# Performance work log

Measured on AMD Instinct MI355X. Metric: run time of the kernel, lower is better.

The kernel has to match this reference:

```python
import jax, jax.numpy as jnp
import numpy as np

N = 64        # n_nodes per graph
H = 128       # hidden channels (128x0e + 128x1o)
NB = 8        # radial bessel basis size
L = 2         # num_interactions
R_MAX = 5.0
AVG_NEIGH = 63.0
DIM = 3       # output vector dim
B = 64        # batch (vmapped)
T = 32        # time-embedding dim
S = 5         # num_species


def _edges(n):
    # fully-connected graph, no self loops (static shapes, jit-friendly)
    s, r = np.meshgrid(np.arange(n), np.arange(n), indexing='ij')
    m = s != r
    return jnp.asarray(s[m]), jnp.asarray(r[m])


def setup_inputs() -> dict:
    key = jax.random.key(0)
    ks = jax.random.split(key, 12)
    sc = 0.05
    return {
        'positions': jax.random.normal(ks[0], (B, N, 3), jnp.float32),
        'node_features': jax.random.randint(ks[1], (B, N), 0, S).astype(jnp.int64),
        'global_features': jax.random.normal(ks[2], (B, T), jnp.float32),
        'emb': jax.random.normal(ks[3], (S, H), jnp.float32) * sc,
        'Wt': jax.random.normal(ks[4], (T, H), jnp.float32) * sc,
        'Wr1': jax.random.normal(ks[5], (L, NB, H), jnp.float32) * sc,
        'Wr2': jax.random.normal(ks[6], (L, H, H), jnp.float32) * sc,
        'Wupd': jax.random.normal(ks[7], (L, H, H), jnp.float32) * sc,
        'Wmix': jax.random.normal(ks[8], (L, H, H), jnp.float32) * sc,
        'Wg1': jax.random.normal(ks[9], (H, H), jnp.float32) * sc,
        'Wg2': jax.random.normal(ks[10], (H, H), jnp.float32) * sc,
        'final_scaling': jnp.ones((), jnp.float32),
    }


def _call_single(pos, z, t, emb, Wt, Wr1, Wr2, Wupd, Wmix, Wg1, Wg2, final_scaling):
    snd, rcv = _edges(N)
    ev = pos[rcv] - pos[snd]                               # [E,3] edge vectors (gather)
    r = jnp.sqrt(jnp.sum(ev * ev, axis=-1) + 1e-12)        # [E]
    u = ev / r[:, None]                                    # unit directions
    # Bessel radial basis with cosine cutoff (r_max acts as soft radius graph)
    n = jnp.arange(1, NB + 1, dtype=pos.dtype)
    rb = jnp.sin(n * jnp.pi * r[:, None] / R_MAX) / r[:, None]   # [E,NB]
    fc = 0.5 * (jnp.cos(jnp.pi * r / R_MAX) + 1.0) * (r < R_MAX)
    rb = rb * fc[:, None]
    # node embedding from species + time embedding
    h = emb[z] + t @ Wt                                    # [N,H] scalar features
    v = jnp.zeros((N, H, DIM), pos.dtype)                  # vector (1o) features
    for l in range(L):
        w = jax.nn.silu(rb @ Wr1[l]) @ Wr2[l]              # [E,H] radial weights
        m0 = w * h[snd]                                    # [E,H] scalar messages
        m1 = m0[:, :, None] * u[:, None, :]                # [E,H,3] vector messages
        a0 = jax.ops.segment_sum(m0, rcv, num_segments=N) / AVG_NEIGH
        a1 = jax.ops.segment_sum(m1, rcv, num_segments=N) / AVG_NEIGH
        h = h + a0 @ Wupd[l]
        v = v + jnp.einsum('ngd,gh->nhd', a1, Wmix[l])
    # equivariant readout: scalar gate per channel contracts vector channels
    g = jax.nn.silu(h @ Wg1) @ Wg2                         # [N,H]
    out = jnp.einsum('nhd,nh->nd', v, g)                   # [N,3]
    return out * final_scaling


def reference(positions, node_features, global_features, emb, Wt, Wr1, Wr2, Wupd, Wmix, Wg1, Wg2, final_scaling):
    f = lambda p, z, t: _call_single(p, z, t, emb, Wt, Wr1, Wr2, Wupd, Wmix, Wg1, Wg2, final_scaling)
    return jax.vmap(f)(positions, node_features, global_features)
```

## Files before the change

### kernel.cpp

```cpp
#include <hip/hip_runtime.h>
#include <math.h>

#define NN 64
#define HH 128
#define NBB 8
#define TT 32
#define BB 64
#define NROW (BB * NN)
#define PLANE ((size_t)NROW * HH)
#define WR1OFF (8 * 16384)

typedef __attribute__((ext_vector_type(8))) short short8;
typedef __attribute__((ext_vector_type(4))) float f32x4;
typedef __attribute__((ext_vector_type(2))) float f32x2;

__device__ __forceinline__ float silu_f(float x) {
  return x * __builtin_amdgcn_rcpf(1.0f + __expf(-x));
}

__device__ __forceinline__ unsigned short f2bf(float x) {
  union { float f; unsigned u; } v; v.f = x;
  unsigned r = v.u + 0x7FFFu + ((v.u >> 16) & 1u);
  return (unsigned short)(r >> 16);
}

__device__ __forceinline__ void gemm16(
    const unsigned short (*sA)[136], const unsigned short* __restrict__ Bp,
    int w, int nlo, int quad, f32x4 C[2]) {
  short8 afr[4];
#pragma unroll
  for (int kt = 0; kt < 4; ++kt)
    afr[kt] = *(const short8*)&sA[nlo][kt * 32 + quad * 8];
#pragma unroll
  for (int nt = 0; nt < 2; ++nt)
#pragma unroll
    for (int kt = 0; kt < 4; ++kt) {
      short8 bfr = *(const short8*)&Bp[((kt * 128 + w * 32 + nt * 16 + nlo) * 4 + quad) * 8];
      C[nt] = __builtin_amdgcn_mfma_f32_16x16x32_bf16(afr[kt], bfr, C[nt], 0, 0, 0);
    }
}

__global__ __launch_bounds__(256) void k_init(
    const float* __restrict__ emb, const int* __restrict__ z,
    const float* __restrict__ gf, const float* __restrict__ Wt,
    const float* __restrict__ Wr1, const float* __restrict__ Wr2,
    const float* __restrict__ Wupd, const float* __restrict__ Wmix,
    const float* __restrict__ Wg1, const float* __restrict__ Wg2,
    float* __restrict__ h, unsigned short* __restrict__ Wpack) {
  __shared__ float tvec[HH];
  __shared__ int sz[NN];
  int b = blockIdx.x, tid = threadIdx.x;
#pragma unroll
  for (int ii = 0; ii < 8; ++ii) {
    int idx = b * 2048 + ii * 256 + tid;
    int m = idx >> 14;
    int local = idx & 16383;
    float val;
    if (m < 2) val = Wr2[idx];
    else if (m < 4) val = Wupd[idx - 32768];
    else if (m < 6) val = Wmix[idx - 65536];
    else if (m == 6) val = Wg1[local];
    else val = Wg2[local];
    int k = local >> 7, n = local & 127;
    int kt = k >> 5, q = (k >> 3) & 3, j = k & 7;
    Wpack[(idx & ~16383) + (((kt * 128 + n) * 4 + q) * 8) + j] = f2bf(val);
  }
  if (tid < 128) {
    int e = b * 128 + tid;
    int l = e >> 12, p = e & 4095;
    int n = p >> 5, q = (p >> 3) & 3, j = p & 7;
    float val = (q == 0) ? Wr1[l * NBB * HH + j * HH + n] : 0.f;
    Wpack[WR1OFF + l * 4096 + p] = f2bf(val);
  }
  if (tid < NN) sz[tid] = z[b * NN + tid];
  if (tid < HH) {
    float acc = 0.f;
#pragma unroll
    for (int k = 0; k < TT; ++k) acc += gf[b * TT + k] * Wt[k * HH + tid];
    tvec[tid] = acc;
  }
  __syncthreads();
  for (int i = tid; i < NN * HH; i += 256) {
    int n = i >> 7, c = i & 127;
    h[(size_t)b * NN * HH + i] = emb[sz[n] * HH + c] + tvec[c];
  }
}

__global__ __launch_bounds__(256) void k_layer(
    const float* __restrict__ pos,
    const float* __restrict__ hin,
    float* __restrict__ ap,
    const unsigned short* __restrict__ Wpack,
    int l) {
  __shared__ __align__(16) unsigned short sh_S[2][NN][136];
  __shared__ __align__(16) unsigned short sh_rbh[2][NN][8];
  __shared__ __align__(16) float sh_u[2][3][NN];

  int blk = blockIdx.x;
  int b = blk >> 5, rp = blk & 31;
  int r0 = rp * 2;
  int tid = threadIdx.x;
  int w = tid >> 6, lane = tid & 63;
  int nlo = lane & 15, quad = lane >> 4;
  const float* hb = hin + (size_t)b * NN * HH;

  float hbv[4][2][4];
#pragma unroll
  for (int mt = 0; mt < 4; ++mt)
#pragma unroll
    for (int nt = 0; nt < 2; ++nt)
#pragma unroll
      for (int reg = 0; reg < 4; ++reg)
        hbv[mt][nt][reg] = hb[(mt * 16 + quad * 4 + reg) * HH + w * 32 + nt * 16 + nlo];

  {
    int s = tid & 63;
    int ksel = (tid >> 6) & 1;
    int ri = (tid >> 7) & 1;
    int r = r0 + ri;
    const float* pb = pos + b * NN * 3;
    float dx = pb[r * 3 + 0] - pb[s * 3 + 0];
    float dy = pb[r * 3 + 1] - pb[s * 3 + 1];
    float dz = pb[r * 3 + 2] - pb[s * 3 + 2];
    float rr = sqrtf(dx * dx + dy * dy + dz * dz + 1e-12f);
    float inv = __builtin_amdgcn_rcpf(rr);
    if (ksel == 0) {
      sh_u[ri][0][s] = dx * inv; sh_u[ri][1][s] = dy * inv; sh_u[ri][2][s] = dz * inv;
    }
    const float PI_OVER_5 = 0.628318530717958647692f;
    float fc = (s != r && rr < 5.0f) ? 0.5f * (__cosf(PI_OVER_5 * rr) + 1.0f) : 0.0f;
    float base = PI_OVER_5 * rr;
    float sc = inv * fc;
    int k0 = ksel * 4;
    float v0 = __sinf((float)(k0 + 1) * base) * sc;
    float v1 = __sinf((float)(k0 + 2) * base) * sc;
    float v2 = __sinf((float)(k0 + 3) * base) * sc;
    float v3 = __sinf((float)(k0 + 4) * base) * sc;
    *(unsigned*)&sh_rbh[ri][s][k0]     = (unsigned)f2bf(v0) | ((unsigned)f2bf(v1) << 16);
    *(unsigned*)&sh_rbh[ri][s][k0 + 2] = (unsigned)f2bf(v2) | ((unsigned)f2bf(v3) << 16);
  }
  __syncthreads();

  {
    const unsigned short* Wr1p = Wpack + WR1OFF + l * 4096;
    short8 bw[2];
#pragma unroll
    for (int nt = 0; nt < 2; ++nt)
      bw[nt] = *(const short8*)&Wr1p[((w * 32 + nt * 16 + nlo) * 4 + quad) * 8];
    const short8 zero8 = {0, 0, 0, 0, 0, 0, 0, 0};
#pragma unroll
    for (int ri = 0; ri < 2; ++ri)
#pragma unroll
      for (int mtp = 0; mtp < 2; ++mtp) {
        f32x4 Cs[2][2];
#pragma unroll
        for (int mi = 0; mi < 2; ++mi)
#pragma unroll
          for (int nt = 0; nt < 2; ++nt) Cs[mi][nt] = (f32x4){0.f, 0.f, 0.f, 0.f};
#pragma unroll
        for (int mi = 0; mi < 2; ++mi) {
          int mt = mtp * 2 + mi;
          short8 afr = (quad == 0) ? *(const short8*)&sh_rbh[ri][mt * 16 + nlo][0] : zero8;
#pragma unroll
          for (int nt = 0; nt < 2; ++nt)
            Cs[mi][nt] = __builtin_amdgcn_mfma_f32_16x16x32_bf16(afr, bw[nt], Cs[mi][nt], 0, 0, 0);
        }
#pragma unroll
        for (int mi = 0; mi < 2; ++mi)
#pragma unroll
          for (int nt = 0; nt < 2; ++nt)
#pragma unroll
            for (int reg = 0; reg < 4; ++reg) {
              int s = (mtp * 2 + mi) * 16 + quad * 4 + reg;
              int c = w * 32 + nt * 16 + nlo;
              sh_S[ri][s][c] = f2bf(silu_f(Cs[mi][nt][reg]));
            }
      }
  }
  __syncthreads();

  const unsigned short* Bbase = Wpack + l * 16384;
  short8 bfr[4][2];
#pragma unroll
  for (int kt = 0; kt < 4; ++kt)
#pragma unroll
    for (int nt = 0; nt < 2; ++nt)
      bfr[kt][nt] = *(const short8*)&Bbase[((kt * 128 + w * 32 + nt * 16 + nlo) * 4 + quad) * 8];

  const float invAvg = 1.0f / 63.0f;
#pragma unroll
  for (int ri = 0; ri < 2; ++ri) {
    float acc0[2] = {0.f, 0.f};
    float a1x[2] = {0.f, 0.f};
    float a1y[2] = {0.f, 0.f};
    float a1z[2] = {0.f, 0.f};
#pragma unroll
    for (int mt = 0; mt < 4; ++mt) {
      short8 afr[4];
      int s_a = mt * 16 + nlo;
#pragma unroll
      for (int kt = 0; kt < 4; ++kt)
        afr[kt] = *(const short8*)&sh_S[ri][s_a][kt * 32 + quad * 8];
      float ux[4], uy[4], uz[4];
#pragma unroll
      for (int reg = 0; reg < 4; ++reg) {
        int s = mt * 16 + quad * 4 + reg;
        ux[reg] = sh_u[ri][0][s]; uy[reg] = sh_u[ri][1][s]; uz[reg] = sh_u[ri][2][s];
      }
#pragma unroll
      for (int nt = 0; nt < 2; ++nt) {
        f32x4 C = {0.f, 0.f, 0.f, 0.f};
#pragma unroll
        for (int kt = 0; kt < 4; ++kt)
          C = __builtin_amdgcn_mfma_f32_16x16x32_bf16(afr[kt], bfr[kt][nt], C, 0, 0, 0);
#pragma unroll
        for (int reg = 0; reg < 4; ++reg) {
          float m0 = C[reg] * hbv[mt][nt][reg];
          acc0[nt] += m0;
          a1x[nt] += m0 * ux[reg];
          a1y[nt] += m0 * uy[reg];
          a1z[nt] += m0 * uz[reg];
        }
      }
    }
#pragma unroll
    for (int nt = 0; nt < 2; ++nt) {
      float q0 = acc0[nt], q1 = a1x[nt], q2 = a1y[nt], q3 = a1z[nt];
      q0 += __shfl_xor(q0, 16); q0 += __shfl_xor(q0, 32);
      q1 += __shfl_xor(q1, 16); q1 += __shfl_xor(q1, 32);
      q2 += __shfl_xor(q2, 16); q2 += __shfl_xor(q2, 32);
      q3 += __shfl_xor(q3, 16); q3 += __shfl_xor(q3, 32);
      if (quad == 0) {
        size_t base = (size_t)(b * NN + r0 + ri) * HH + w * 32 + nt * 16 + nlo;
        ap[base]             = q0 * invAvg;
        ap[PLANE + base]     = q1 * invAvg;
        ap[2 * PLANE + base] = q2 * invAvg;
        ap[3 * PLANE + base] = q3 * invAvg;
      }
    }
  }
}

__global__ __launch_bounds__(256) void k_update(
    const float* __restrict__ ap, const float* __restrict__ hin,
    float* __restrict__ hout, float* __restrict__ vp,
    const unsigned short* __restrict__ Wpack) {
  __shared__ __align__(16) unsigned short sh_a[4][16][136];
  int tid = threadIdx.x, w = tid >> 6, lane = tid & 63;
  int nlo = lane & 15, quad = lane >> 4;
  int row0 = blockIdx.x * 16;
#pragma unroll
  for (int p = 0; p < 4; ++p)
#pragma unroll
    for (int ii = 0; ii < 4; ++ii) {
      int i = ii * 256 + tid;
      int rr = i >> 6, c2 = (i & 63) * 2;
      f32x2 t = *(const f32x2*)&ap[p * PLANE + (size_t)(row0 + rr) * HH + c2];
      *(unsigned*)&sh_a[p][rr][c2] = (unsigned)f2bf(t.x) | ((unsigned)f2bf(t.y) << 16);
    }
  __syncthreads();
  f32x4 Ch[2] = {{0,0,0,0},{0,0,0,0}}, Cx[2] = {{0,0,0,0},{0,0,0,0}};
  f32x4 Cy[2] = {{0,0,0,0},{0,0,0,0}}, Cz[2] = {{0,0,0,0},{0,0,0,0}};
  gemm16(sh_a[0], Wpack + 2 * 16384, w, nlo, quad, Ch);
  gemm16(sh_a[1], Wpack + 4 * 16384, w, nlo, quad, Cx);
  gemm16(sh_a[2], Wpack + 4 * 16384, w, nlo, quad, Cy);
  gemm16(sh_a[3], Wpack + 4 * 16384, w, nlo, quad, Cz);
#pragma unroll
  for (int nt = 0; nt < 2; ++nt)
#pragma unroll
    for (int reg = 0; reg < 4; ++reg) {
      size_t row = row0 + quad * 4 + reg;
      int col = w * 32 + nt * 16 + nlo;
      hout[row * HH + col] = hin[row * HH + col] + Ch[nt][reg];
      vp[0 * PLANE + row * HH + col] = Cx[nt][reg];
      vp[1 * PLANE + row * HH + col] = Cy[nt][reg];
      vp[2 * PLANE + row * HH + col] = Cz[nt][reg];
    }
}

__global__ __launch_bounds__(256) void k_update_ro(
    const float* __restrict__ ap, const float* __restrict__ hin,
    const float* __restrict__ vp,
    const unsigned short* __restrict__ Wpack,
    const float* __restrict__ fs, float* __restrict__ out) {
  __shared__ __align__(16) unsigned short sh_a[4][16][136];
  __shared__ __align__(16) unsigned short sh_h[16][136];
  __shared__ float red[4][16][3];
  int tid = threadIdx.x, w = tid >> 6, lane = tid & 63;
  int nlo = lane & 15, quad = lane >> 4;
  int row0 = blockIdx.x * 16;
#pragma unroll
  for (int p = 0; p < 4; ++p)
#pragma unroll
    for (int ii = 0; ii < 4; ++ii) {
      int i = ii * 256 + tid;
      int rr = i >> 6, c2 = (i & 63) * 2;
      f32x2 t = *(const f32x2*)&ap[p * PLANE + (size_t)(row0 + rr) * HH + c2];
      *(unsigned*)&sh_a[p][rr][c2] = (unsigned)f2bf(t.x) | ((unsigned)f2bf(t.y) << 16);
    }
  __syncthreads();
  f32x4 Ch[2] = {{0,0,0,0},{0,0,0,0}}, Cx[2] = {{0,0,0,0},{0,0,0,0}};
  f32x4 Cy[2] = {{0,0,0,0},{0,0,0,0}}, Cz[2] = {{0,0,0,0},{0,0,0,0}};
  gemm16(sh_a[0], Wpack + 3 * 16384, w, nlo, quad, Ch);
  gemm16(sh_a[1], Wpack + 5 * 16384, w, nlo, quad, Cx);
  gemm16(sh_a[2], Wpack + 5 * 16384, w, nlo, quad, Cy);
  gemm16(sh_a[3], Wpack + 5 * 16384, w, nlo, quad, Cz);
#pragma unroll
  for (int nt = 0; nt < 2; ++nt)
#pragma unroll
    for (int reg = 0; reg < 4; ++reg) {
      int rl = quad * 4 + reg;
      size_t row = row0 + rl;
      int col = w * 32 + nt * 16 + nlo;
      sh_h[rl][col] = f2bf(hin[row * HH + col] + Ch[nt][reg]);
      Cx[nt][reg] += vp[0 * PLANE + row * HH + col];
      Cy[nt][reg] += vp[1 * PLANE + row * HH + col];
      Cz[nt][reg] += vp[2 * PLANE + row * HH + col];
    }
  __syncthreads();
  unsigned short (*sh_q)[136] = sh_a[0];
  f32x4 Cq[2] = {{0,0,0,0},{0,0,0,0}};
  gemm16(sh_h, Wpack + 6 * 16384, w, nlo, quad, Cq);
#pragma unroll
  for (int nt = 0; nt < 2; ++nt)
#pragma unroll
    for (int reg = 0; reg < 4; ++reg)
      sh_q[quad * 4 + reg][w * 32 + nt * 16 + nlo] = f2bf(silu_f(Cq[nt][reg]));
  __syncthreads();
  f32x4 Cg[2] = {{0,0,0,0},{0,0,0,0}};
  gemm16(sh_q, Wpack + 7 * 16384, w, nlo, quad, Cg);
  float pr[3][4];
#pragma unroll
  for (int d = 0; d < 3; ++d)
#pragma unroll
    for (int reg = 0; reg < 4; ++reg) pr[d][reg] = 0.f;
#pragma unroll
  for (int nt = 0; nt < 2; ++nt)
#pragma unroll
    for (int reg = 0; reg < 4; ++reg) {
      float gv = Cg[nt][reg];
      pr[0][reg] += gv * Cx[nt][reg];
      pr[1][reg] += gv * Cy[nt][reg];
      pr[2][reg] += gv * Cz[nt][reg];
    }
#pragma unroll
  for (int off = 1; off < 16; off <<= 1)
#pragma unroll
    for (int d = 0; d < 3; ++d)
#pragma unroll
      for (int reg = 0; reg < 4; ++reg)
        pr[d][reg] += __shfl_xor(pr[d][reg], off);
  if (nlo == 0) {
#pragma unroll
    for (int d = 0; d < 3; ++d)
#pragma unroll
      for (int reg = 0; reg < 4; ++reg)
        red[w][quad * 4 + reg][d] = pr[d][reg];
  }
  __syncthreads();
  if (tid < 48) {
    int row = tid / 3, d = tid % 3;
    float s = red[0][row][d] + red[1][row][d] + red[2][row][d] + red[3][row][d];
    out[(size_t)(row0 + row) * 3 + d] = s * fs[0];
  }
}

extern "C" void kernel_launch(void* const* d_in, const int* in_sizes, int n_in,
                              void* d_out, int out_size, void* d_ws, size_t ws_size,
                              hipStream_t stream) {
  const float* pos  = (const float*)d_in[0];
  const int*   z    = (const int*)d_in[1];
  const float* gf   = (const float*)d_in[2];
  const float* emb  = (const float*)d_in[3];
  const float* Wt   = (const float*)d_in[4];
  const float* Wr1  = (const float*)d_in[5];
  const float* Wr2  = (const float*)d_in[6];
  const float* Wupd = (const float*)d_in[7];
  const float* Wmix = (const float*)d_in[8];
  const float* Wg1  = (const float*)d_in[9];
  const float* Wg2  = (const float*)d_in[10];
  const float* fs   = (const float*)d_in[11];
  float* out = (float*)d_out;

  float* ws = (float*)d_ws;
  float* hA = ws;
  float* hB = ws + PLANE;
  float* vp = ws + 2 * PLANE;
  float* apl = ws + 5 * PLANE;
  unsigned short* Wpack = (unsigned short*)(ws + 9 * PLANE);

  k_init<<<dim3(BB), dim3(256), 0, stream>>>(emb, z, gf, Wt, Wr1, Wr2, Wupd,
                                             Wmix, Wg1, Wg2, hA, Wpack);
  k_layer<<<dim3(BB * 32), dim3(256), 0, stream>>>(pos, hA, apl, Wpack, 0);
  k_update<<<dim3(256), dim3(256), 0, stream>>>(apl, hA, hB, vp, Wpack);
  k_layer<<<dim3(BB * 32), dim3(256), 0, stream>>>(pos, hB, apl, Wpack, 1);
  k_update_ro<<<dim3(256), dim3(256), 0, stream>>>(apl, hB, vp, Wpack, fs, out);
}
```

Measured before the change: 155.6 us.

## Eliminate intermediate update kernel by recomputing h in layer and deferring vector mix

Removes the k_update launch. The layer-1 kernel now recomputes h = hA + a0·Wupd0 per block with MFMA from bf16 layer-0 aggregates. The layer-0 vector mix is deferred to the final readout, which sums both layers' Wmix contributions by linearity. Aggregates are stored as bf16 instead of fp32, halving that traffic and dropping the fp32 v-plane round trip. The cost is redundant recomputation of the 64x128x128 h-update in each of the 32 blocks per graph, plus extra bf16 rounding of aggregates.

```diff
diff --git a/kernel.cpp b/kernel.cpp
--- a/kernel.cpp
+++ b/kernel.cpp
@@ -88,8 +88,9 @@
 
 __global__ __launch_bounds__(256) void k_layer(
     const float* __restrict__ pos,
-    const float* __restrict__ hin,
-    float* __restrict__ ap,
+    const float* __restrict__ hA,
+    const unsigned short* __restrict__ a0in,
+    unsigned short* __restrict__ apout,
     const unsigned short* __restrict__ Wpack,
     int l) {
   __shared__ __align__(16) unsigned short sh_S[2][NN][136];
@@ -102,16 +103,16 @@
   int tid = threadIdx.x;
   int w = tid >> 6, lane = tid & 63;
   int nlo = lane & 15, quad = lane >> 4;
-  const float* hb = hin + (size_t)b * NN * HH;
-
-  float hbv[4][2][4];
+
+  f32x4 hbv[4][2];
 #pragma unroll
   for (int mt = 0; mt < 4; ++mt)
 #pragma unroll
     for (int nt = 0; nt < 2; ++nt)
 #pragma unroll
       for (int reg = 0; reg < 4; ++reg)
-        hbv[mt][nt][reg] = hb[(mt * 16 + quad * 4 + reg) * HH + w * 32 + nt * 16 + nlo];
+        hbv[mt][nt][reg] =
+            hA[((size_t)b * NN + mt * 16 + quad * 4 + reg) * HH + w * 32 + nt * 16 + nlo];
 
   {
     int s = tid & 63;
@@ -139,7 +140,33 @@
     *(unsigned*)&sh_rbh[ri][s][k0]     = (unsigned)f2bf(v0) | ((unsigned)f2bf(v1) << 16);
     *(unsigned*)&sh_rbh[ri][s][k0 + 2] = (unsigned)f2bf(v2) | ((unsigned)f2bf(v3) << 16);
   }
-  __syncthreads();
+  if (l) {
+    for (int i = tid; i < NN * 64; i += 256) {
+      int s = i >> 6, c2 = (i & 63) * 2;
+      *(unsigned*)&sh_S[0][s][c2] =
+          *(const unsigned*)&a0in[((size_t)b * NN + s) * HH + c2];
+    }
+  }
+  __syncthreads();
+
+  if (l) {
+    const unsigned short* Bu = Wpack + 2 * 16384;
+#pragma unroll
+    for (int mt = 0; mt < 4; ++mt) {
+      short8 afr[4];
+#pragma unroll
+      for (int kt = 0; kt < 4; ++kt)
+        afr[kt] = *(const short8*)&sh_S[0][mt * 16 + nlo][kt * 32 + quad * 8];
+#pragma unroll
+      for (int nt = 0; nt < 2; ++nt)
+#pragma unroll
+        for (int kt = 0; kt < 4; ++kt) {
+          short8 bfr = *(const short8*)&Bu[((kt * 128 + w * 32 + nt * 16 + nlo) * 4 + quad) * 8];
+          hbv[mt][nt] = __builtin_amdgcn_mfma_f32_16x16x32_bf16(afr[kt], bfr, hbv[mt][nt], 0, 0, 0);
+        }
+    }
+    __syncthreads();
+  }
 
   {
     const unsigned short* Wr1p = Wpack + WR1OFF + l * 4096;
@@ -232,91 +259,57 @@
       q3 += __shfl_xor(q3, 16); q3 += __shfl_xor(q3, 32);
       if (quad == 0) {
         size_t base = (size_t)(b * NN + r0 + ri) * HH + w * 32 + nt * 16 + nlo;
-        ap[base]             = q0 * invAvg;
-        ap[PLANE + base]     = q1 * invAvg;
-        ap[2 * PLANE + base] = q2 * invAvg;
-        ap[3 * PLANE + base] = q3 * invAvg;
+        apout[(l * 4 + 0) * PLANE + base] = f2bf(q0 * invAvg);
+        apout[(l * 4 + 1) * PLANE + base] = f2bf(q1 * invAvg);
+        apout[(l * 4 + 2) * PLANE + base] = f2bf(q2 * invAvg);
+        apout[(l * 4 + 3) * PLANE + base] = f2bf(q3 * invAvg);
       }
     }
   }
 }
 
-__global__ __launch_bounds__(256) void k_update(
-    const float* __restrict__ ap, const float* __restrict__ hin,
-    float* __restrict__ hout, float* __restrict__ vp,
-    const unsigned short* __restrict__ Wpack) {
-  __shared__ __align__(16) unsigned short sh_a[4][16][136];
-  int tid = threadIdx.x, w = tid >> 6, lane = tid & 63;
-  int nlo = lane & 15, quad = lane >> 4;
-  int row0 = blockIdx.x * 16;
-#pragma unroll
-  for (int p = 0; p < 4; ++p)
-#pragma unroll
-    for (int ii = 0; ii < 4; ++ii) {
-      int i = ii * 256 + tid;
-      int rr = i >> 6, c2 = (i & 63) * 2;
-      f32x2 t = *(const f32x2*)&ap[p * PLANE + (size_t)(row0 + rr) * HH + c2];
-      *(unsigned*)&sh_a[p][rr][c2] = (unsigned)f2bf(t.x) | ((unsigned)f2bf(t.y) << 16);
-    }
-  __syncthreads();
-  f32x4 Ch[2] = {{0,0,0,0},{0,0,0,0}}, Cx[2] = {{0,0,0,0},{0,0,0,0}};
-  f32x4 Cy[2] = {{0,0,0,0},{0,0,0,0}}, Cz[2] = {{0,0,0,0},{0,0,0,0}};
-  gemm16(sh_a[0], Wpack + 2 * 16384, w, nlo, quad, Ch);
-  gemm16(sh_a[1], Wpack + 4 * 16384, w, nlo, quad, Cx);
-  gemm16(sh_a[2], Wpack + 4 * 16384, w, nlo, quad, Cy);
-  gemm16(sh_a[3], Wpack + 4 * 16384, w, nlo, quad, Cz);
-#pragma unroll
-  for (int nt = 0; nt < 2; ++nt)
-#pragma unroll
-    for (int reg = 0; reg < 4; ++reg) {
-      size_t row = row0 + quad * 4 + reg;
-      int col = w * 32 + nt * 16 + nlo;
-      hout[row * HH + col] = hin[row * HH + col] + Ch[nt][reg];
-      vp[0 * PLANE + row * HH + col] = Cx[nt][reg];
-      vp[1 * PLANE + row * HH + col] = Cy[nt][reg];
-      vp[2 * PLANE + row * HH + col] = Cz[nt][reg];
-    }
-}
-
 __global__ __launch_bounds__(256) void k_update_ro(
-    const float* __restrict__ ap, const float* __restrict__ hin,
-    const float* __restrict__ vp,
+    const unsigned short* __restrict__ apbf, const float* __restrict__ hA,
     const unsigned short* __restrict__ Wpack,
     const float* __restrict__ fs, float* __restrict__ out) {
-  __shared__ __align__(16) unsigned short sh_a[4][16][136];
+  __shared__ __align__(16) unsigned short sh_a[8][16][136];
   __shared__ __align__(16) unsigned short sh_h[16][136];
   __shared__ float red[4][16][3];
   int tid = threadIdx.x, w = tid >> 6, lane = tid & 63;
   int nlo = lane & 15, quad = lane >> 4;
   int row0 = blockIdx.x * 16;
 #pragma unroll
-  for (int p = 0; p < 4; ++p)
+  for (int p = 0; p < 8; ++p)
 #pragma unroll
     for (int ii = 0; ii < 4; ++ii) {
       int i = ii * 256 + tid;
       int rr = i >> 6, c2 = (i & 63) * 2;
-      f32x2 t = *(const f32x2*)&ap[p * PLANE + (size_t)(row0 + rr) * HH + c2];
-      *(unsigned*)&sh_a[p][rr][c2] = (unsigned)f2bf(t.x) | ((unsigned)f2bf(t.y) << 16);
-    }
-  __syncthreads();
-  f32x4 Ch[2] = {{0,0,0,0},{0,0,0,0}}, Cx[2] = {{0,0,0,0},{0,0,0,0}};
-  f32x4 Cy[2] = {{0,0,0,0},{0,0,0,0}}, Cz[2] = {{0,0,0,0},{0,0,0,0}};
-  gemm16(sh_a[0], Wpack + 3 * 16384, w, nlo, quad, Ch);
-  gemm16(sh_a[1], Wpack + 5 * 16384, w, nlo, quad, Cx);
-  gemm16(sh_a[2], Wpack + 5 * 16384, w, nlo, quad, Cy);
-  gemm16(sh_a[3], Wpack + 5 * 16384, w, nlo, quad, Cz);
-#pragma unroll
-  for (int nt = 0; nt < 2; ++nt)
-#pragma unroll
-    for (int reg = 0; reg < 4; ++reg) {
-      int rl = quad * 4 + reg;
-      size_t row = row0 + rl;
-      int col = w * 32 + nt * 16 + nlo;
-      sh_h[rl][col] = f2bf(hin[row * HH + col] + Ch[nt][reg]);
-      Cx[nt][reg] += vp[0 * PLANE + row * HH + col];
-      Cy[nt][reg] += vp[1 * PLANE + row * HH + col];
-      Cz[nt][reg] += vp[2 * PLANE + row * HH + col];
-    }
+      *(unsigned*)&sh_a[p][rr][c2] =
+          *(const unsigned*)&apbf[p * PLANE + (size_t)(row0 + rr) * HH + c2];
+    }
+  f32x4 Ch[2];
+#pragma unroll
+  for (int nt = 0; nt < 2; ++nt)
+#pragma unroll
+    for (int reg = 0; reg < 4; ++reg)
+      Ch[nt][reg] = hA[(size_t)(row0 + quad * 4 + reg) * HH + w * 32 + nt * 16 + nlo];
+  __syncthreads();
+  gemm16(sh_a[0], Wpack + 2 * 16384, w, nlo, quad, Ch);
+  gemm16(sh_a[4], Wpack + 3 * 16384, w, nlo, quad, Ch);
+  f32x4 Cx[2] = {{0,0,0,0},{0,0,0,0}};
+  f32x4 Cy[2] = {{0,0,0,0},{0,0,0,0}};
+  f32x4 Cz[2] = {{0,0,0,0},{0,0,0,0}};
+  gemm16(sh_a[1], Wpack + 4 * 16384, w, nlo, quad, Cx);
+  gemm16(sh_a[5], Wpack + 5 * 16384, w, nlo, quad, Cx);
+  gemm16(sh_a[2], Wpack + 4 * 16384, w, nlo, quad, Cy);
+  gemm16(sh_a[6], Wpack + 5 * 16384, w, nlo, quad, Cy);
+  gemm16(sh_a[3], Wpack + 4 * 16384, w, nlo, quad, Cz);
+  gemm16(sh_a[7], Wpack + 5 * 16384, w, nlo, quad, Cz);
+#pragma unroll
+  for (int nt = 0; nt < 2; ++nt)
+#pragma unroll
+    for (int reg = 0; reg < 4; ++reg)
+      sh_h[quad * 4 + reg][w * 32 + nt * 16 + nlo] = f2bf(Ch[nt][reg]);
   __syncthreads();
   unsigned short (*sh_q)[136] = sh_a[0];
   f32x4 Cq[2] = {{0,0,0,0},{0,0,0,0}};
@@ -384,15 +377,12 @@
 
   float* ws = (float*)d_ws;
   float* hA = ws;
-  float* hB = ws + PLANE;
-  float* vp = ws + 2 * PLANE;
-  float* apl = ws + 5 * PLANE;
-  unsigned short* Wpack = (unsigned short*)(ws + 9 * PLANE);
+  unsigned short* apbf = (unsigned short*)(ws + PLANE);
+  unsigned short* Wpack = (unsigned short*)(ws + 5 * PLANE);
 
   k_init<<<dim3(BB), dim3(256), 0, stream>>>(emb, z, gf, Wt, Wr1, Wr2, Wupd,
                                              Wmix, Wg1, Wg2, hA, Wpack);
-  k_layer<<<dim3(BB * 32), dim3(256), 0, stream>>>(pos, hA, apl, Wpack, 0);
-  k_update<<<dim3(256), dim3(256), 0, stream>>>(apl, hA, hB, vp, Wpack);
-  k_layer<<<dim3(BB * 32), dim3(256), 0, stream>>>(pos, hB, apl, Wpack, 1);
-  k_update_ro<<<dim3(256), dim3(256), 0, stream>>>(apl, hB, vp, Wpack, fs, out);
-}
+  k_layer<<<dim3(BB * 32), dim3(256), 0, stream>>>(pos, hA, apbf, apbf, Wpack, 0);
+  k_layer<<<dim3(BB * 32), dim3(256), 0, stream>>>(pos, hA, apbf, apbf, Wpack, 1);
+  k_update_ro<<<dim3(256), dim3(256), 0, stream>>>(apbf, hA, Wpack, fs, out);
+}
```

After: 156.1 us. Within noise of the previous version (+0.3%).
